# Performance work log

Hardware: AMD Instinct MI355X
Metric: run time of the kernel (lower is better)

## Reference

```python
import jax, jax.numpy as jnp
import numpy as np

N = 20000        # total nodes (cells + genes)
N_GENES = 2000   # gene nodes = last N_GENES node ids (edge sources)
E = 640000       # edges
EMB = 128        # emb_dim
ED = 32          # edge_dim
PD = 64          # P.shape[1]
OUT = 16         # out_dim
L_RUN = 2        # n_layers - 1 convs actually run (zip with edge_update_fns[1:])


def _lin_init(key, fan_in, fan_out):
    kw, kb = jax.random.split(key)
    bound = 1.0 / np.sqrt(fan_in)
    W = jax.random.uniform(kw, (fan_in, fan_out), jnp.float32, -bound, bound)
    b = jax.random.uniform(kb, (fan_out,), jnp.float32, -bound, bound)
    return W, b


def setup_inputs() -> dict:
    key = jax.random.key(0)
    ks = jax.random.split(key, 16)
    x = jax.random.normal(ks[0], (N, N_GENES), jnp.float32)
    edge_attr = jax.random.normal(ks[1], (E, ED), jnp.float32)
    # bipartite: sources are gene nodes (last N_GENES ids), targets any node
    src = jax.random.randint(ks[2], (E,), N - N_GENES, N, jnp.int32)
    dst = jax.random.randint(ks[3], (E,), 0, N, jnp.int32)
    edge_index = jnp.stack([src, dst], axis=0)  # [2, E]

    W_emb, b_emb = _lin_init(ks[4], N_GENES, EMB)
    msg_Ws, msg_bs, upd_Ws, upd_bs = [], [], [], []
    for l in range(L_RUN):
        mW, mb = _lin_init(ks[5 + l], EMB + ED, PD)
        uW, ub = _lin_init(ks[7 + l], PD + EMB, EMB)
        msg_Ws.append(mW); msg_bs.append(mb); upd_Ws.append(uW); upd_bs.append(ub)
    msg_W = jnp.stack(msg_Ws); msg_b = jnp.stack(msg_bs)
    upd_W = jnp.stack(upd_Ws); upd_b = jnp.stack(upd_bs)
    W_node, b_node = _lin_init(ks[9], EMB, OUT)
    W_ep, b_ep = _lin_init(ks[10], 2 * EMB + ED, 1)
    P = jax.random.normal(ks[11], (N_GENES, PD), jnp.float32)
    return {
        'x': x, 'edge_attr': edge_attr, 'edge_index': edge_index,
        'W_emb': W_emb, 'b_emb': b_emb,
        'msg_W': msg_W, 'msg_b': msg_b, 'upd_W': upd_W, 'upd_b': upd_b,
        'W_node': W_node, 'b_node': b_node, 'W_ep': W_ep, 'b_ep': b_ep,
        'P': P,
    }


def reference(x, edge_attr, edge_index, W_emb, b_emb, msg_W, msg_b,
              upd_W, upd_b, W_node, b_node, W_ep, b_ep, P):
    n_nodes = x.shape[0]
    n_genes = W_emb.shape[0]
    src, dst = edge_index[0], edge_index[1]
    # idx = edge_index[0] - (edge_index[0].max() - (n_genes - 1))
    idx = src - (jnp.max(src) - (n_genes - 1))
    Pe = P[idx]  # [E, PD] per-edge lookup

    h = x @ W_emb + b_emb  # [N, EMB]
    n_layers_run = msg_W.shape[0]
    for l in range(n_layers_run):
        # message: relu(Linear(cat(x_j, edge_attr))) * P[idx]
        msg_in = jnp.concatenate([h[src], edge_attr], axis=-1)  # [E, EMB+ED]
        m = jax.nn.relu(msg_in @ msg_W[l] + msg_b[l]) * Pe       # [E, PD]
        # scatter-sum aggregate at target nodes
        aggr = jax.ops.segment_sum(m, dst, num_segments=n_nodes)  # [N, PD]
        # update: relu(Linear(cat(aggr, x)))
        upd_in = jnp.concatenate([aggr, h], axis=-1)              # [N, PD+EMB]
        h = jax.nn.relu(upd_in @ upd_W[l] + upd_b[l])             # [N, EMB]

    node_prediction = h @ W_node + b_node  # [N, OUT]
    ep_in = jnp.concatenate([h[src], h[dst], edge_attr], axis=-1)  # [E, 2*EMB+ED]
    edge_prediction = ep_in @ W_ep + b_ep  # [E, 1]
    return node_prediction, edge_prediction
```

## Files before the change

### kernel.cpp

```cpp
#include <hip/hip_runtime.h>
#include <hip/hip_bf16.h>

typedef float f32x4 __attribute__((ext_vector_type(4)));

#define N_NODES 20000
#define NGENES  2000
#define NEDGE   640000
#define EMB     128
#define ED      32
#define PD      64
#define OUTD    16
#define KEMB    2000

__global__ __launch_bounds__(256) void k_prep(const int* __restrict__ src,
                                              const int* __restrict__ dst,
                                              int* __restrict__ smax,
                                              int* __restrict__ cnt) {
    __shared__ int sm[256];
    int i = blockIdx.x * 256 + threadIdx.x;
    int s = src[i];
    atomicAdd(&cnt[dst[i]], 1);
    sm[threadIdx.x] = s;
    __syncthreads();
    for (int st = 128; st > 0; st >>= 1) {
        if (threadIdx.x < st) sm[threadIdx.x] = max(sm[threadIdx.x], sm[threadIdx.x + st]);
        __syncthreads();
    }
    if (threadIdx.x == 0) atomicMax(smax, sm[0]);
}

__global__ __launch_bounds__(256) void k_srcmax(const int* __restrict__ src,
                                                int* __restrict__ out) {
    __shared__ int sm[256];
    int i = blockIdx.x * 256 + threadIdx.x;
    sm[threadIdx.x] = (i < NEDGE) ? src[i] : 0;
    __syncthreads();
    for (int s = 128; s > 0; s >>= 1) {
        if (threadIdx.x < s) sm[threadIdx.x] = max(sm[threadIdx.x], sm[threadIdx.x + s]);
        __syncthreads();
    }
    if (threadIdx.x == 0) atomicMax(out, sm[0]);
}

__global__ __launch_bounds__(1024) void k_scan(const int* __restrict__ cnt,
                                               int* __restrict__ row_start,
                                               int* __restrict__ cursor) {
    __shared__ int a[1024], b[1024];
    __shared__ int carry_s;
    int tid = threadIdx.x;
    if (tid == 0) carry_s = 0;
    __syncthreads();
    for (int chunk = 0; chunk < (N_NODES + 1023) / 1024; ++chunk) {
        int i = chunk * 1024 + tid;
        int v = (i < N_NODES) ? cnt[i] : 0;
        a[tid] = v;
        __syncthreads();
        int* s_ = a; int* d_ = b;
        for (int off = 1; off < 1024; off <<= 1) {
            int val = s_[tid];
            if (tid >= off) val += s_[tid - off];
            d_[tid] = val;
            __syncthreads();
            int* t = s_; s_ = d_; d_ = t;
        }
        int incl = s_[tid];
        int carry = carry_s;
        if (i < N_NODES) {
            row_start[i + 1] = carry + incl;
            cursor[i] = carry + incl - v;
        }
        __syncthreads();
        if (tid == 1023) carry_s = carry + incl;
        __syncthreads();
    }
    if (tid == 0) row_start[0] = 0;
}

__global__ __launch_bounds__(256) void k_scatter(const int* __restrict__ dst,
                                                 int* __restrict__ cursor,
                                                 int* __restrict__ perm) {
    int e = blockIdx.x * 256 + threadIdx.x;
    int pos = atomicAdd(&cursor[dst[e]], 1);
    perm[pos] = e;
}

__global__ __launch_bounds__(256) void k_gather(const float* __restrict__ ea,
                                                const int* __restrict__ src,
                                                const int* __restrict__ perm,
                                                float* __restrict__ ea_s,
                                                int* __restrict__ src_s) {
    int i = blockIdx.x * 256 + threadIdx.x;
    int e = perm[i];
    src_s[i] = src[e];
    const f32x4* a = (const f32x4*)(ea + (long)e * ED);
    f32x4* o = (f32x4*)(ea_s + (long)i * ED);
#pragma unroll
    for (int c = 0; c < 8; ++c) o[c] = a[c];
}

__global__ __launch_bounds__(256) void k_emb_part(const float* __restrict__ x,
                                                  const float* __restrict__ W,
                                                  float* __restrict__ hpart) {
    __shared__ float As[64 * 17];
    __shared__ float Bs[16 * 64];
    int tid = threadIdx.x;
    int b = blockIdx.x;
    int ks = b & 3, nt = (b >> 2) & 1, mt = b >> 3;
    int row0 = mt * 64, n0 = nt * 64;
    int kt0 = ks * 32, kt1 = min(125, kt0 + 32);
    int tx = tid & 15, ty = tid >> 4;
    float acc[4][4] = {};
    int ar = tid >> 2, ac = (tid & 3) * 4;
    int bkr = tid >> 4, bc = (tid & 15) * 4;
    for (int kt = kt0; kt < kt1; ++kt) {
        int k0 = kt * 16;
        if (row0 + ar < N_NODES) {
            f32x4 av = *(const f32x4*)(x + (long)(row0 + ar) * KEMB + k0 + ac);
#pragma unroll
            for (int j = 0; j < 4; ++j) As[ar * 17 + ac + j] = av[j];
        } else {
#pragma unroll
            for (int j = 0; j < 4; ++j) As[ar * 17 + ac + j] = 0.f;
        }
        *(f32x4*)(Bs + bkr * 64 + bc) = *(const f32x4*)(W + (long)(k0 + bkr) * EMB + n0 + bc);
        __syncthreads();
#pragma unroll 1
        for (int kk = 0; kk < 16; ++kk) {
            float a[4];
#pragma unroll
            for (int i = 0; i < 4; ++i) a[i] = As[(ty * 4 + i) * 17 + kk];
            f32x4 bv = *(const f32x4*)(Bs + kk * 64 + tx * 4);
#pragma unroll
            for (int i = 0; i < 4; ++i)
#pragma unroll
                for (int j = 0; j < 4; ++j) acc[i][j] += a[i] * bv[j];
        }
        __syncthreads();
    }
    float* hp = hpart + (size_t)ks * N_NODES * EMB;
#pragma unroll
    for (int i = 0; i < 4; ++i) {
        int row = row0 + ty * 4 + i;
        if (row >= N_NODES) continue;
        f32x4 o;
#pragma unroll
        for (int j = 0; j < 4; ++j) o[j] = acc[i][j];
        *(f32x4*)(hp + (long)row * EMB + n0 + tx * 4) = o;
    }
}

__global__ __launch_bounds__(256) void k_emb_reduce(const float* __restrict__ hpart,
                                                    const float* __restrict__ bias,
                                                    float* __restrict__ h) {
    long i = (long)blockIdx.x * 256 + threadIdx.x;
    long p = i * 4;
    int c = (int)(p & 127);
    f32x4 a0 = *(const f32x4*)(hpart + p);
    f32x4 a1 = *(const f32x4*)(hpart + (size_t)N_NODES * EMB + p);
    f32x4 a2 = *(const f32x4*)(hpart + 2 * (size_t)N_NODES * EMB + p);
    f32x4 a3 = *(const f32x4*)(hpart + 3 * (size_t)N_NODES * EMB + p);
    f32x4 bb = *(const f32x4*)(bias + c);
    f32x4 o;
#pragma unroll
    for (int j = 0; j < 4; ++j) o[j] = (a0[j] + a1[j]) + (a2[j] + a3[j]) + bb[j];
    *(f32x4*)(h + p) = o;
}

__global__ __launch_bounds__(256) void k_emb_f32(const float* __restrict__ x,
                                                 const float* __restrict__ W,
                                                 const float* __restrict__ bias,
                                                 float* __restrict__ h) {
    __shared__ float As[64 * 17];
    __shared__ float Bs[16 * 64];
    int tid = threadIdx.x;
    int mt = blockIdx.x >> 1, nt = blockIdx.x & 1;
    int row0 = mt * 64, n0 = nt * 64;
    int tx = tid & 15, ty = tid >> 4;
    float acc[4][4] = {};
    int ar = tid >> 2, ac = (tid & 3) * 4;
    int bkr = tid >> 4, bc = (tid & 15) * 4;
    for (int kt = 0; kt < 125; ++kt) {
        int k0 = kt * 16;
        if (row0 + ar < N_NODES) {
            f32x4 av = *(const f32x4*)(x + (long)(row0 + ar) * KEMB + k0 + ac);
#pragma unroll
            for (int j = 0; j < 4; ++j) As[ar * 17 + ac + j] = av[j];
        } else {
#pragma unroll
            for (int j = 0; j < 4; ++j) As[ar * 17 + ac + j] = 0.f;
        }
        *(f32x4*)(Bs + bkr * 64 + bc) = *(const f32x4*)(W + (long)(k0 + bkr) * EMB + n0 + bc);
        __syncthreads();
#pragma unroll 1
        for (int kk = 0; kk < 16; ++kk) {
            float a[4];
#pragma unroll
            for (int i = 0; i < 4; ++i) a[i] = As[(ty * 4 + i) * 17 + kk];
            f32x4 bv = *(const f32x4*)(Bs + kk * 64 + tx * 4);
#pragma unroll
            for (int i = 0; i < 4; ++i)
#pragma unroll
                for (int j = 0; j < 4; ++j) acc[i][j] += a[i] * bv[j];
        }
        __syncthreads();
    }
#pragma unroll
    for (int i = 0; i < 4; ++i) {
        int row = row0 + ty * 4 + i;
        if (row >= N_NODES) continue;
        f32x4 o;
#pragma unroll
        for (int j = 0; j < 4; ++j) o[j] = acc[i][j] + bias[n0 + tx * 4 + j];
        *(f32x4*)(h + (long)row * EMB + n0 + tx * 4) = o;
    }
}

__global__ __launch_bounds__(256) void k_gene(const float* __restrict__ h,
                                              const float* __restrict__ mW,
                                              const float* __restrict__ mb,
                                              const int* __restrict__ smax,
                                              float* __restrict__ G) {
    __shared__ float Ws[128 * 64];
    __shared__ float hs[4][128];
    int tid = threadIdx.x;
    for (int i = tid; i < 2048; i += 256)
        *(f32x4*)(Ws + i * 4) = *(const f32x4*)(mW + i * 4);
    int base = *smax - (NGENES - 1);
    int g0 = blockIdx.x * 4;
    for (int i = tid; i < 128; i += 256) {
        int r = i >> 5, c = (i & 31) * 4;
        *(f32x4*)(&hs[r][c]) = *(const f32x4*)(h + (long)(base + g0 + r) * EMB + c);
    }
    __syncthreads();
    int wv = tid >> 6, lane = tid & 63;
    float a0 = mb[lane], a1 = 0.f, a2 = 0.f, a3 = 0.f;
#pragma unroll 8
    for (int k = 0; k < 128; k += 4) {
        a0 += hs[wv][k + 0] * Ws[(k + 0) * 64 + lane];
        a1 += hs[wv][k + 1] * Ws[(k + 1) * 64 + lane];
        a2 += hs[wv][k + 2] * Ws[(k + 2) * 64 + lane];
        a3 += hs[wv][k + 3] * Ws[(k + 3) * 64 + lane];
    }
    G[(long)(g0 + wv) * PD + lane] = (a0 + a1) + (a2 + a3);
}

__global__ __launch_bounds__(256) void k_fusedagg(const float* __restrict__ G,
                                                  const float* __restrict__ mW,
                                                  const float* __restrict__ P,
                                                  const float* __restrict__ ea_s,
                                                  const int* __restrict__ src_s,
                                                  const int* __restrict__ row_start,
                                                  const int* __restrict__ smax,
                                                  float* __restrict__ aggr) {
    int tid = threadIdx.x;
    int wv = tid >> 6, lane = tid & 63;
    float we[32];
#pragma unroll
    for (int k = 0; k < 32; ++k) we[k] = mW[(long)(128 + k) * PD + lane];
    int base = *smax - (NGENES - 1);
    int n = blockIdx.x * 4 + wv;
    int j0 = row_start[n], j1 = row_start[n + 1];
    float acc = 0.f;
    for (int j = j0; j < j1; ++j) {
        int g = src_s[j] - base;
        const f32x4* er = (const f32x4*)(ea_s + (long)j * ED);
        f32x4 ev[8];
#pragma unroll
        for (int c = 0; c < 8; ++c) ev[c] = er[c];
        float t0 = G[(long)g * PD + lane], t1 = 0.f, t2 = 0.f, t3 = 0.f;
#pragma unroll
        for (int c = 0; c < 8; ++c) {
            t0 += ev[c][0] * we[c * 4 + 0];
            t1 += ev[c][1] * we[c * 4 + 1];
            t2 += ev[c][2] * we[c * 4 + 2];
            t3 += ev[c][3] * we[c * 4 + 3];
        }
        float t = (t0 + t1) + (t2 + t3);
        acc += fmaxf(t, 0.f) * P[(long)g * PD + lane];
    }
    aggr[(long)n * PD + lane] = acc;
}

__global__ __launch_bounds__(256) void k_msg_f32(const float* __restrict__ h,
                                                 const float* __restrict__ ea,
                                                 const int* __restrict__ src,
                                                 const int* __restrict__ dst,
                                                 const float* __restrict__ mW,
                                                 const float* __restrict__ mb,
                                                 const float* __restrict__ P,
                                                 const int* __restrict__ smax,
                                                 float* __restrict__ aggr) {
    int e = blockIdx.x * 256 + threadIdx.x;
    int s = src[e], d = dst[e];
    float acc[PD];
#pragma unroll
    for (int o = 0; o < PD; ++o) acc[o] = mb[o];
#pragma unroll 1
    for (int kb = 0; kb < 10; ++kb) {
        float in[16];
        if (kb < 8) {
            f32x4 v0 = *(const f32x4*)(h + (long)s * EMB + kb * 16);
            f32x4 v1 = *(const f32x4*)(h + (long)s * EMB + kb * 16 + 4);
            f32x4 v2 = *(const f32x4*)(h + (long)s * EMB + kb * 16 + 8);
            f32x4 v3 = *(const f32x4*)(h + (long)s * EMB + kb * 16 + 12);
#pragma unroll
            for (int j = 0; j < 4; ++j) { in[j] = v0[j]; in[4+j] = v1[j]; in[8+j] = v2[j]; in[12+j] = v3[j]; }
        } else {
            f32x4 v0 = *(const f32x4*)(ea + (long)e * ED + (kb - 8) * 16);
            f32x4 v1 = *(const f32x4*)(ea + (long)e * ED + (kb - 8) * 16 + 4);
            f32x4 v2 = *(const f32x4*)(ea + (long)e * ED + (kb - 8) * 16 + 8);
            f32x4 v3 = *(const f32x4*)(ea + (long)e * ED + (kb - 8) * 16 + 12);
#pragma unroll
            for (int j = 0; j < 4; ++j) { in[j] = v0[j]; in[4+j] = v1[j]; in[8+j] = v2[j]; in[12+j] = v3[j]; }
        }
#pragma unroll 1
        for (int kk = 0; kk < 16; ++kk) {
            const float* wrow = mW + (long)(kb * 16 + kk) * PD;
            float v = in[kk];
#pragma unroll
            for (int o = 0; o < PD; ++o) acc[o] += v * wrow[o];
        }
    }
    int base = *smax - (NGENES - 1);
    const float* Pe = P + (long)(s - base) * PD;
    float* arow = aggr + (long)d * PD;
#pragma unroll
    for (int o = 0; o < PD; ++o) {
        float v = fmaxf(acc[o], 0.f) * Pe[o];
        unsafeAtomicAdd(arow + o, v);
    }
}

__global__ __launch_bounds__(512) void k_upd_f32(const float* __restrict__ aggr,
                                                 float* __restrict__ h,
                                                 const float* __restrict__ uW,
                                                 const float* __restrict__ ub)
{
    __shared__ float lds[64 * 193];
    int tid = threadIdx.x;
    int n0 = blockIdx.x * 64;
    for (int i = tid; i < 64 * 64; i += 512) {
        int nl = i >> 6, k = i & 63;
        lds[nl * 193 + k] = (n0 + nl < N_NODES) ? aggr[(long)(n0 + nl) * PD + k] : 0.f;
    }
    for (int i = tid; i < 64 * 128; i += 512) {
        int nl = i >> 7, k = i & 127;
        lds[nl * 193 + 64 + k] = (n0 + nl < N_NODES) ? h[(long)(n0 + nl) * EMB + k] : 0.f;
    }
    __syncthreads();
    int wv = tid >> 6, l = tid & 63;
    int o0 = wv * 16;
    int n = n0 + l;
    float acc[16];
#pragma unroll
    for (int o = 0; o < 16; ++o) acc[o] = ub[o0 + o];
#pragma unroll 4
    for (int k = 0; k < 192; ++k) {
        float v = lds[l * 193 + k];
        const float* wrow = uW + (long)k * EMB + o0;
#pragma unroll
        for (int o = 0; o < 16; ++o) acc[o] += v * wrow[o];
    }
    if (n < N_NODES) {
#pragma unroll
        for (int c = 0; c < 4; ++c) {
            f32x4 v;
#pragma unroll
            for (int j = 0; j < 4; ++j) v[j] = fmaxf(acc[c * 4 + j], 0.f);
            *(f32x4*)(h + (long)n * EMB + o0 + c * 4) = v;
        }
    }
}

__global__ __launch_bounds__(256) void k_node_pn(const float* __restrict__ h,
                                                 const float* __restrict__ W,
                                                 const float* __restrict__ b,
                                                 const float* __restrict__ Wep,
                                                 float* __restrict__ out,
                                                 float* __restrict__ pn1,
                                                 float* __restrict__ pn2) {
    int n = blockIdx.x * 256 + threadIdx.x;
    if (n >= N_NODES) return;
    float acc[OUTD];
#pragma unroll
    for (int o = 0; o < OUTD; ++o) acc[o] = b[o];
    float p1a = 0.f, p1b = 0.f, p2a = 0.f, p2b = 0.f;
#pragma unroll 1
    for (int kb = 0; kb < 32; ++kb) {
        f32x4 hv = *(const f32x4*)(h + (long)n * EMB + kb * 4);
#pragma unroll
        for (int j = 0; j < 4; ++j) {
            const float* wrow = W + (long)(kb * 4 + j) * OUTD;
#pragma unroll
            for (int o = 0; o < OUTD; ++o) acc[o] += hv[j] * wrow[o];
        }
        p1a += hv[0] * Wep[kb * 4 + 0] + hv[1] * Wep[kb * 4 + 1];
        p1b += hv[2] * Wep[kb * 4 + 2] + hv[3] * Wep[kb * 4 + 3];
        p2a += hv[0] * Wep[128 + kb * 4 + 0] + hv[1] * Wep[128 + kb * 4 + 1];
        p2b += hv[2] * Wep[128 + kb * 4 + 2] + hv[3] * Wep[128 + kb * 4 + 3];
    }
#pragma unroll
    for (int c = 0; c < 4; ++c) {
        f32x4 v;
#pragma unroll
        for (int j = 0; j < 4; ++j) v[j] = acc[c * 4 + j];
        *(f32x4*)(out + (long)n * OUTD + c * 4) = v;
    }
    pn1[n] = p1a + p1b;
    pn2[n] = p2a + p2b;
}

__global__ __launch_bounds__(256) void k_node_f32(const float* __restrict__ h,
                                                  const float* __restrict__ W,
                                                  const float* __restrict__ b,
                                                  float* __restrict__ out) {
    int n = blockIdx.x * 256 + threadIdx.x;
    if (n >= N_NODES) return;
    float acc[OUTD];
#pragma unroll
    for (int o = 0; o < OUTD; ++o) acc[o] = b[o];
#pragma unroll 1
    for (int kb = 0; kb < 32; ++kb) {
        f32x4 hv = *(const f32x4*)(h + (long)n * EMB + kb * 4);
#pragma unroll
        for (int j = 0; j < 4; ++j) {
            const float* wrow = W + (long)(kb * 4 + j) * OUTD;
#pragma unroll
            for (int o = 0; o < OUTD; ++o) acc[o] += hv[j] * wrow[o];
        }
    }
#pragma unroll
    for (int c = 0; c < 4; ++c) {
        f32x4 v;
#pragma unroll
        for (int j = 0; j < 4; ++j) v[j] = acc[c * 4 + j];
        *(f32x4*)(out + (long)n * OUTD + c * 4) = v;
    }
}

__global__ __launch_bounds__(256) void k_edge2(const float* __restrict__ ea,
                                               const int* __restrict__ src,
                                               const int* __restrict__ dstv,
                                               const float* __restrict__ pn1,
                                               const float* __restrict__ pn2,
                                               const float* __restrict__ Wep,
                                               const float* __restrict__ bep,
                                               float* __restrict__ out) {
    int e = blockIdx.x * 256 + threadIdx.x;
    float a0 = bep[0] + pn1[src[e]] + pn2[dstv[e]];
    float a1 = 0.f, a2 = 0.f, a3 = 0.f;
#pragma unroll
    for (int kb = 0; kb < 8; ++kb) {
        f32x4 av = *(const f32x4*)(ea + (long)e * ED + kb * 4);
        a0 += av[0] * Wep[256 + kb * 4 + 0];
        a1 += av[1] * Wep[256 + kb * 4 + 1];
        a2 += av[2] * Wep[256 + kb * 4 + 2];
        a3 += av[3] * Wep[256 + kb * 4 + 3];
    }
    out[e] = (a0 + a1) + (a2 + a3);
}

__global__ __launch_bounds__(256) void k_edge_f32(const float* __restrict__ h,
                                                  const float* __restrict__ ea,
                                                  const int* __restrict__ src,
                                                  const int* __restrict__ dst,
                                                  const float* __restrict__ Wep,
                                                  const float* __restrict__ bep,
                                                  float* __restrict__ out) {
    int e = blockIdx.x * 256 + threadIdx.x;
    int s = src[e], d = dst[e];
    float a0 = bep[0], a1 = 0.f, a2 = 0.f, a3 = 0.f;
#pragma unroll 1
    for (int kb = 0; kb < 32; ++kb) {
        f32x4 hv = *(const f32x4*)(h + (long)s * EMB + kb * 4);
        a0 += hv[0] * Wep[kb * 4 + 0];
        a1 += hv[1] * Wep[kb * 4 + 1];
        a2 += hv[2] * Wep[kb * 4 + 2];
        a3 += hv[3] * Wep[kb * 4 + 3];
    }
#pragma unroll 1
    for (int kb = 0; kb < 32; ++kb) {
        f32x4 hv = *(const f32x4*)(h + (long)d * EMB + kb * 4);
        a0 += hv[0] * Wep[128 + kb * 4 + 0];
        a1 += hv[1] * Wep[128 + kb * 4 + 1];
        a2 += hv[2] * Wep[128 + kb * 4 + 2];
        a3 += hv[3] * Wep[128 + kb * 4 + 3];
    }
#pragma unroll 1
    for (int kb = 0; kb < 8; ++kb) {
        f32x4 av = *(const f32x4*)(ea + (long)e * ED + kb * 4);
        a0 += av[0] * Wep[256 + kb * 4 + 0];
        a1 += av[1] * Wep[256 + kb * 4 + 1];
        a2 += av[2] * Wep[256 + kb * 4 + 2];
        a3 += av[3] * Wep[256 + kb * 4 + 3];
    }
    out[e] = (a0 + a1) + (a2 + a3);
}

extern "C" void kernel_launch(void* const* d_in, const int* in_sizes, int n_in,
                              void* d_out, int out_size, void* d_ws, size_t ws_size,
                              hipStream_t stream) {
    const float* x      = (const float*)d_in[0];
    const float* ea     = (const float*)d_in[1];
    const int*   eidx   = (const int*)d_in[2];
    const float* W_emb  = (const float*)d_in[3];
    const float* b_emb  = (const float*)d_in[4];
    const float* msg_W  = (const float*)d_in[5];
    const float* msg_b  = (const float*)d_in[6];
    const float* upd_W  = (const float*)d_in[7];
    const float* upd_b  = (const float*)d_in[8];
    const float* W_node = (const float*)d_in[9];
    const float* b_node = (const float*)d_in[10];
    const float* W_ep   = (const float*)d_in[11];
    const float* b_ep   = (const float*)d_in[12];
    const float* P      = (const float*)d_in[13];
    float* out = (float*)d_out;

    const int* src = eidx;
    const int* dst = eidx + NEDGE;

    size_t off = 0;
    char* w = (char*)d_ws;
    float* h    = (float*)(w + off); off += (size_t)N_NODES * EMB * 4;
    float* aggr = (float*)(w + off); off += (size_t)N_NODES * PD * 4;
    int*   smax = (int*)(w + off);   off += 16;
    if (ws_size < off) return;

    size_t off2 = off;
    int* cnt       = (int*)(w + off2); off2 += (size_t)N_NODES * 4;
    int* row_start = (int*)(w + off2); off2 += ((size_t)(N_NODES + 1) * 4 + 15) & ~15ull;
    int* cursor    = (int*)(w + off2); off2 += (size_t)N_NODES * 4;
    int* perm      = (int*)(w + off2); off2 += (size_t)NEDGE * 4;
    int* src_s     = (int*)(w + off2); off2 += (size_t)NEDGE * 4;
    float* pn1     = (float*)(w + off2); off2 += (size_t)N_NODES * 4;
    float* pn2     = (float*)(w + off2); off2 += (size_t)N_NODES * 4;
    float* G       = (float*)(w + off2); off2 += (size_t)NGENES * PD * 4;
    float* ea_s    = (float*)(w + off2); off2 += (size_t)NEDGE * ED * 4;
    float* hpart   = (float*)(w + off2); off2 += 4 * (size_t)N_NODES * EMB * 4;
    const bool fast = (ws_size >= off2);

    hipMemsetAsync(smax, 0, 4, stream);

    if (fast) {
        hipMemsetAsync(cnt, 0, (size_t)N_NODES * 4, stream);
        k_prep<<<NEDGE / 256, 256, 0, stream>>>(src, dst, smax, cnt);
        k_scan<<<1, 1024, 0, stream>>>(cnt, row_start, cursor);
        k_scatter<<<NEDGE / 256, 256, 0, stream>>>(dst, cursor, perm);
        k_gather<<<NEDGE / 256, 256, 0, stream>>>(ea, src, perm, ea_s, src_s);

        k_emb_part<<<313 * 8, 256, 0, stream>>>(x, W_emb, hpart);
        k_emb_reduce<<<2500, 256, 0, stream>>>(hpart, b_emb, h);

        k_gene<<<NGENES / 4, 256, 0, stream>>>(h, msg_W, msg_b, smax, G);
        k_fusedagg<<<N_NODES / 4, 256, 0, stream>>>(G, msg_W, P, ea_s, src_s,
                                                    row_start, smax, aggr);
        k_upd_f32<<<313, 512, 0, stream>>>(aggr, h, upd_W, upd_b);
        k_gene<<<NGENES / 4, 256, 0, stream>>>(h, msg_W + 160 * PD, msg_b + PD, smax, G);
        k_fusedagg<<<N_NODES / 4, 256, 0, stream>>>(G, msg_W + 160 * PD, P, ea_s, src_s,
                                                    row_start, smax, aggr);
        k_upd_f32<<<313, 512, 0, stream>>>(aggr, h, upd_W + 192 * EMB, upd_b + EMB);

        k_node_pn<<<(N_NODES + 255) / 256, 256, 0, stream>>>(h, W_node, b_node, W_ep,
                                                             out, pn1, pn2);
        k_edge2<<<NEDGE / 256, 256, 0, stream>>>(ea, src, dst, pn1, pn2, W_ep, b_ep,
                                                 out + (size_t)N_NODES * OUTD);
    } else {
        k_srcmax<<<NEDGE / 256, 256, 0, stream>>>(src, smax);
        k_emb_f32<<<313 * 2, 256, 0, stream>>>(x, W_emb, b_emb, h);
        hipMemsetAsync(aggr, 0, (size_t)N_NODES * PD * 4, stream);
        k_msg_f32<<<NEDGE / 256, 256, 0, stream>>>(h, ea, src, dst, msg_W, msg_b, P, smax, aggr);
        k_upd_f32<<<313, 512, 0, stream>>>(aggr, h, upd_W, upd_b);
        hipMemsetAsync(aggr, 0, (size_t)N_NODES * PD * 4, stream);
        k_msg_f32<<<NEDGE / 256, 256, 0, stream>>>(h, ea, src, dst,
                                                   msg_W + 160 * PD, msg_b + PD, P, smax, aggr);
        k_upd_f32<<<313, 512, 0, stream>>>(aggr, h, upd_W + 192 * EMB, upd_b + EMB);
        k_node_f32<<<(N_NODES + 255) / 256, 256, 0, stream>>>(h, W_node, b_node, out);
        k_edge_f32<<<NEDGE / 256, 256, 0, stream>>>(h, ea, src, dst, W_ep, b_ep,
                                                    out + (size_t)N_NODES * OUTD);
    }
}
```

Baseline: 1.215 ms.

## Split fused edge aggregation into tiled edge-message GEMM plus CSR segment sum

Replaces the per-node fused aggregation kernel with two kernels. The first is a shared-memory tiled GEMM over 64-edge blocks that computes edge_attr times the message weights, adds the gene term G, applies relu and multiplies by P, writing a dense per-edge message buffer. The second sums those messages per destination row using the CSR offsets. The gather kernel that built a sorted edge_attr copy is removed, with src_s now written during the scatter and edge_attr read through perm inside the GEMM. This trades the redundant per-lane edge_attr dot products for an extra E×64 float write and read per layer, and hpart now shares memory with the message buffer.

```diff
diff --git a/kernel.cpp b/kernel.cpp
--- a/kernel.cpp
+++ b/kernel.cpp
@@ -76,26 +76,15 @@
     if (tid == 0) row_start[0] = 0;
 }
 
-__global__ __launch_bounds__(256) void k_scatter(const int* __restrict__ dst,
+__global__ __launch_bounds__(256) void k_scatter(const int* __restrict__ src,
+                                                 const int* __restrict__ dst,
                                                  int* __restrict__ cursor,
-                                                 int* __restrict__ perm) {
+                                                 int* __restrict__ perm,
+                                                 int* __restrict__ src_s) {
     int e = blockIdx.x * 256 + threadIdx.x;
     int pos = atomicAdd(&cursor[dst[e]], 1);
     perm[pos] = e;
-}
-
-__global__ __launch_bounds__(256) void k_gather(const float* __restrict__ ea,
-                                                const int* __restrict__ src,
-                                                const int* __restrict__ perm,
-                                                float* __restrict__ ea_s,
-                                                int* __restrict__ src_s) {
-    int i = blockIdx.x * 256 + threadIdx.x;
-    int e = perm[i];
-    src_s[i] = src[e];
-    const f32x4* a = (const f32x4*)(ea + (long)e * ED);
-    f32x4* o = (f32x4*)(ea_s + (long)i * ED);
-#pragma unroll
-    for (int c = 0; c < 8; ++c) o[c] = a[c];
+    src_s[pos] = src[e];
 }
 
 __global__ __launch_bounds__(256) void k_emb_part(const float* __restrict__ x,
@@ -244,41 +233,73 @@
     G[(long)(g0 + wv) * PD + lane] = (a0 + a1) + (a2 + a3);
 }
 
-__global__ __launch_bounds__(256) void k_fusedagg(const float* __restrict__ G,
-                                                  const float* __restrict__ mW,
-                                                  const float* __restrict__ P,
-                                                  const float* __restrict__ ea_s,
-                                                  const int* __restrict__ src_s,
-                                                  const int* __restrict__ row_start,
-                                                  const int* __restrict__ smax,
-                                                  float* __restrict__ aggr) {
+__global__ __launch_bounds__(256) void k_msgmat(const float* __restrict__ ea,
+                                                const int* __restrict__ perm,
+                                                const int* __restrict__ src_s,
+                                                const float* __restrict__ mW,
+                                                const float* __restrict__ G,
+                                                const float* __restrict__ P,
+                                                const int* __restrict__ smax,
+                                                float* __restrict__ m) {
+    __shared__ float EA[64 * 33];
+    __shared__ float Ws[32 * 64];
     int tid = threadIdx.x;
-    int wv = tid >> 6, lane = tid & 63;
-    float we[32];
-#pragma unroll
-    for (int k = 0; k < 32; ++k) we[k] = mW[(long)(128 + k) * PD + lane];
+    int e0 = blockIdx.x * 64;
+    for (int i = tid; i < 512; i += 256)
+        *(f32x4*)(Ws + i * 4) = *(const f32x4*)(mW + 128 * 64 + i * 4);
+    for (int i = tid; i < 512; i += 256) {
+        int r = i >> 3, c = (i & 7) * 4;
+        int e = perm[e0 + r];
+        f32x4 v = *(const f32x4*)(ea + (long)e * ED + c);
+        EA[r * 33 + c + 0] = v[0];
+        EA[r * 33 + c + 1] = v[1];
+        EA[r * 33 + c + 2] = v[2];
+        EA[r * 33 + c + 3] = v[3];
+    }
+    __syncthreads();
+    int tx = tid & 15, ty = tid >> 4;
+    float acc[4][4] = {};
+#pragma unroll
+    for (int k = 0; k < 32; ++k) {
+        float a[4];
+#pragma unroll
+        for (int i = 0; i < 4; ++i) a[i] = EA[(ty * 4 + i) * 33 + k];
+        f32x4 bv = *(const f32x4*)(Ws + k * 64 + tx * 4);
+#pragma unroll
+        for (int i = 0; i < 4; ++i)
+#pragma unroll
+            for (int j = 0; j < 4; ++j) acc[i][j] += a[i] * bv[j];
+    }
     int base = *smax - (NGENES - 1);
-    int n = blockIdx.x * 4 + wv;
+#pragma unroll
+    for (int i = 0; i < 4; ++i) {
+        int j = e0 + ty * 4 + i;
+        int g = src_s[j] - base;
+        f32x4 Gv = *(const f32x4*)(G + (long)g * PD + tx * 4);
+        f32x4 Pv = *(const f32x4*)(P + (long)g * PD + tx * 4);
+        f32x4 o;
+#pragma unroll
+        for (int jj = 0; jj < 4; ++jj)
+            o[jj] = fmaxf(acc[i][jj] + Gv[jj], 0.f) * Pv[jj];
+        *(f32x4*)(m + (long)j * PD + tx * 4) = o;
+    }
+}
+
+__global__ __launch_bounds__(256) void k_sumagg(const float* __restrict__ m,
+                                                const int* __restrict__ row_start,
+                                                float* __restrict__ aggr) {
+    int n = blockIdx.x * 4 + (threadIdx.x >> 6);
+    int lane = threadIdx.x & 63;
+    if (n >= N_NODES) return;
     int j0 = row_start[n], j1 = row_start[n + 1];
-    float acc = 0.f;
-    for (int j = j0; j < j1; ++j) {
-        int g = src_s[j] - base;
-        const f32x4* er = (const f32x4*)(ea_s + (long)j * ED);
-        f32x4 ev[8];
-#pragma unroll
-        for (int c = 0; c < 8; ++c) ev[c] = er[c];
-        float t0 = G[(long)g * PD + lane], t1 = 0.f, t2 = 0.f, t3 = 0.f;
-#pragma unroll
-        for (int c = 0; c < 8; ++c) {
-            t0 += ev[c][0] * we[c * 4 + 0];
-            t1 += ev[c][1] * we[c * 4 + 1];
-            t2 += ev[c][2] * we[c * 4 + 2];
-            t3 += ev[c][3] * we[c * 4 + 3];
-        }
-        float t = (t0 + t1) + (t2 + t3);
-        acc += fmaxf(t, 0.f) * P[(long)g * PD + lane];
-    }
-    aggr[(long)n * PD + lane] = acc;
+    float acc0 = 0.f, acc1 = 0.f;
+    int j = j0;
+    for (; j + 1 < j1; j += 2) {
+        acc0 += m[(long)j * PD + lane];
+        acc1 += m[(long)(j + 1) * PD + lane];
+    }
+    if (j < j1) acc0 += m[(long)j * PD + lane];
+    aggr[(long)n * PD + lane] = acc0 + acc1;
 }
 
 __global__ __launch_bounds__(256) void k_msg_f32(const float* __restrict__ h,
@@ -535,8 +556,8 @@
     float* pn1     = (float*)(w + off2); off2 += (size_t)N_NODES * 4;
     float* pn2     = (float*)(w + off2); off2 += (size_t)N_NODES * 4;
     float* G       = (float*)(w + off2); off2 += (size_t)NGENES * PD * 4;
-    float* ea_s    = (float*)(w + off2); off2 += (size_t)NEDGE * ED * 4;
-    float* hpart   = (float*)(w + off2); off2 += 4 * (size_t)N_NODES * EMB * 4;
+    float* m       = (float*)(w + off2); off2 += (size_t)NEDGE * PD * 4;
+    float* hpart   = m;
     const bool fast = (ws_size >= off2);
 
     hipMemsetAsync(smax, 0, 4, stream);
@@ -545,19 +566,18 @@
         hipMemsetAsync(cnt, 0, (size_t)N_NODES * 4, stream);
         k_prep<<<NEDGE / 256, 256, 0, stream>>>(src, dst, smax, cnt);
         k_scan<<<1, 1024, 0, stream>>>(cnt, row_start, cursor);
-        k_scatter<<<NEDGE / 256, 256, 0, stream>>>(dst, cursor, perm);
-        k_gather<<<NEDGE / 256, 256, 0, stream>>>(ea, src, perm, ea_s, src_s);
+        k_scatter<<<NEDGE / 256, 256, 0, stream>>>(src, dst, cursor, perm, src_s);
 
         k_emb_part<<<313 * 8, 256, 0, stream>>>(x, W_emb, hpart);
         k_emb_reduce<<<2500, 256, 0, stream>>>(hpart, b_emb, h);
 
         k_gene<<<NGENES / 4, 256, 0, stream>>>(h, msg_W, msg_b, smax, G);
-        k_fusedagg<<<N_NODES / 4, 256, 0, stream>>>(G, msg_W, P, ea_s, src_s,
-                                                    row_start, smax, aggr);
+        k_msgmat<<<NEDGE / 64, 256, 0, stream>>>(ea, perm, src_s, msg_W, G, P, smax, m);
+        k_sumagg<<<N_NODES / 4, 256, 0, stream>>>(m, row_start, aggr);
         k_upd_f32<<<313, 512, 0, stream>>>(aggr, h, upd_W, upd_b);
         k_gene<<<NGENES / 4, 256, 0, stream>>>(h, msg_W + 160 * PD, msg_b + PD, smax, G);
-        k_fusedagg<<<N_NODES / 4, 256, 0, stream>>>(G, msg_W + 160 * PD, P, ea_s, src_s,
-                                                    row_start, smax, aggr);
+        k_msgmat<<<NEDGE / 64, 256, 0, stream>>>(ea, perm, src_s, msg_W + 160 * PD, G, P, smax, m);
+        k_sumagg<<<N_NODES / 4, 256, 0, stream>>>(m, row_start, aggr);
         k_upd_f32<<<313, 512, 0, stream>>>(aggr, h, upd_W + 192 * EMB, upd_b + EMB);
 
         k_node_pn<<<(N_NODES + 255) / 256, 256, 0, stream>>>(h, W_node, b_node, W_ep,
```

Result: faster. 995.9 us (-18.1%).
